# Performance work log

Hardware: AMD Instinct MI355X
Metric: run time of the kernel (lower is better)

Reference implementation:

```python
import jax, jax.numpy as jnp
import numpy as np
from jax import lax

B, T, IN_DIM, HIDDEN = 8, 4096, 1024, 1024


def setup_inputs() -> dict:
    key = jax.random.key(0)
    k_x, k_wd, k_wb = jax.random.split(key, 3)
    x = jax.random.normal(k_x, (B, T, IN_DIM), dtype=jnp.float32)
    h0 = jnp.zeros((B, HIDDEN), dtype=jnp.float32)
    # nn.Linear default init ~ U(-1/sqrt(in), 1/sqrt(in)); b_proj.weight ~ N(0, 0.02)
    lim = 1.0 / np.sqrt(IN_DIM)
    Wd = jax.random.uniform(k_wd, (HIDDEN, IN_DIM), jnp.float32, -lim, lim)
    bd = jnp.zeros((HIDDEN,), dtype=jnp.float32)
    Wb = 0.02 * jax.random.normal(k_wb, (HIDDEN, IN_DIM), dtype=jnp.float32)
    bb = jnp.zeros((HIDDEN,), dtype=jnp.float32)
    # 'hasani' init: A_log = log(linspace(0.5, 2.0, hidden))
    A_log = jnp.log(jnp.linspace(0.5, 2.0, HIDDEN, dtype=jnp.float32))
    return {"x": x, "h0": h0, "Wd": Wd, "bd": bd, "Wb": Wb, "bb": bb, "A_log": A_log}


def _combine(c1, c2):
    # composition of affine maps h -> a*h + b
    a1, b1 = c1
    a2, b2 = c2
    return a1 * a2, a2 * b1 + b2


def reference(x, h0, Wd, bd, Wb, bb, A_log):
    # projections: (B,T,in) @ (in,hidden)
    delta = jax.nn.softplus(jnp.einsum('bti,hi->bth', x, Wd) + bd)
    b_t = delta * (jnp.einsum('bti,hi->bth', x, Wb) + bb)
    A = jnp.exp(A_log)                      # (H,) decay rate
    A_t = jnp.exp(-delta * A)               # (B,T,H)
    # parallel (Blelloch/Heinsen-style) associative scan over T:
    # cumulative affine maps give h_t = A_cum_t * h0 + B_cum_t
    A_cum, B_cum = lax.associative_scan(_combine, (A_t, b_t), axis=1)
    h_full = A_cum * h0[:, None, :] + B_cum  # (B,T,H)
    return jnp.tanh(h_full)                  # bound=True
```

## Files before the change

kernel.cpp:

```cpp
#include <hip/hip_runtime.h>
#include <math.h>

#define B_DIM 8
#define T_DIM 4096
#define K_DIM 1024
#define H_DIM 1024
#define M_DIM (B_DIM * T_DIM)

#define CH 64
#define NC (T_DIM / CH)
#define BK 64
#define NKS (K_DIM / BK)

typedef short bf16x8 __attribute__((ext_vector_type(8)));
typedef float f32x4  __attribute__((ext_vector_type(4)));

__device__ __forceinline__ unsigned short f2bf(float f) {
  unsigned int u = __builtin_bit_cast(unsigned int, f);
  u += 0x7FFFu + ((u >> 16) & 1u);
  return (unsigned short)(u >> 16);
}

__device__ __forceinline__ void gload_lds16(const void* g, void* l) {
  __builtin_amdgcn_global_load_lds(
      (const __attribute__((address_space(1))) unsigned int*)g,
      (__attribute__((address_space(3))) unsigned int*)l,
      16 , 0 , 0 );
}

__device__ __forceinline__ float softplus_fast(float x) {
  float e = __expf(-fabsf(x));
  return fmaxf(x, 0.f) + __logf(1.f + e);
}

__device__ __forceinline__ float tanh_fast(float x) {
  float e = __expf(2.f * x);
  return 1.f - 2.f * __builtin_amdgcn_rcpf(e + 1.f);
}

__global__ __launch_bounds__(256) void k_cvt(const float* __restrict__ in,
                                             unsigned short* __restrict__ out,
                                             int n8) {
  int i = blockIdx.x * 256 + threadIdx.x;
  if (i >= n8) return;
  float4 v0 = ((const float4*)in)[i * 2 + 0];
  float4 v1 = ((const float4*)in)[i * 2 + 1];
  bf16x8 r;
  r[0] = (short)f2bf(v0.x); r[1] = (short)f2bf(v0.y);
  r[2] = (short)f2bf(v0.z); r[3] = (short)f2bf(v0.w);
  r[4] = (short)f2bf(v1.x); r[5] = (short)f2bf(v1.y);
  r[6] = (short)f2bf(v1.z); r[7] = (short)f2bf(v1.w);
  ((bf16x8*)out)[i] = r;
}

#define MFMA_Q(AF, BF, MQ, NQ)                                                 \
  do {                                                                         \
    __builtin_amdgcn_s_setprio(1);                                             \
    _Pragma("unroll")                                                          \
    for (int mm = 0; mm < 4; mm++)                                             \
      _Pragma("unroll")                                                        \
      for (int nn = 0; nn < 2; nn++)                                           \
        _Pragma("unroll")                                                      \
        for (int kk = 0; kk < 2; kk++)                                         \
          acc[(MQ)*4 + mm][(NQ)*2 + nn] =                                      \
              __builtin_amdgcn_mfma_f32_16x16x32_bf16(                         \
                  AF[mm*2 + kk], BF[nn*2 + kk],                                \
                  acc[(MQ)*4 + mm][(NQ)*2 + nn], 0, 0, 0);                     \
    __builtin_amdgcn_s_setprio(0);                                             \
  } while (0)

__global__ __launch_bounds__(512, 2) void k_gemm_dual(
    const unsigned short* __restrict__ Xb,
    const unsigned short* __restrict__ Wdb,
    const unsigned short* __restrict__ Wbb,
    const float* __restrict__ bd,
    const float* __restrict__ bb,
    const float* __restrict__ A_log,
    float* __restrict__ a_out,
    float* __restrict__ b_out,
    float* __restrict__ aggA,
    float* __restrict__ aggB)
{
  __shared__ unsigned short As[2][256 * BK];
  __shared__ unsigned short Bs[2][256 * BK];

  const int tid  = threadIdx.x;
  const int wgid = blockIdx.x;
  const int xcd  = wgid & 7;
  const int j    = wgid >> 3;
  const int bm   = (xcd * 16 + (j >> 3)) * 256;
  const int bn   = (j & 7) * 128;

  const int w    = tid >> 6;
  const int lane = tid & 63;
  const int wm   = (w >> 2) * 128;
  const int wq   = w & 3;
  const int wn   = wq * 64;

  f32x4 acc[8][4];
  const f32x4 z4 = {0.f, 0.f, 0.f, 0.f};
#pragma unroll
  for (int m = 0; m < 8; m++)
#pragma unroll
    for (int n = 0; n < 4; n++) acc[m][n] = z4;

  const int fr = lane & 15;
  const int hi = lane >> 4;

  auto stage = [&](int t, int d) {
    const int k0 = t * BK;
#pragma unroll
    for (int i = 0; i < 4; i++) {
      int idx = i * 512 + tid;
      int row = idx >> 3;
      int cg  = (idx & 7) ^ (row & 7);
      size_t ga = (size_t)(bm + row) * K_DIM + (size_t)(k0 + cg * 8);
      gload_lds16(Xb + ga, (char*)As[d] + idx * 16);
      int h = bn + (row >> 6) * 32 + (row & 31);
      const unsigned short* Wsrc = (row & 32) ? Wbb : Wdb;
      size_t gb = (size_t)h * K_DIM + (size_t)(k0 + cg * 8);
      gload_lds16(Wsrc + gb, (char*)Bs[d] + idx * 16);
    }
  };

  auto readA = [&](int d, int mq, bf16x8* Af) {
#pragma unroll
    for (int mm = 0; mm < 4; mm++) {
      int row = wm + mq * 64 + mm * 16 + fr;
#pragma unroll
      for (int kk = 0; kk < 2; kk++) {
        int ch = (kk * 4 + hi) ^ (row & 7);
        Af[mm * 2 + kk] = *(const bf16x8*)&As[d][row * BK + ch * 8];
      }
    }
  };
  auto readB = [&](int d, int nq, bf16x8* Bf) {
#pragma unroll
    for (int nn = 0; nn < 2; nn++) {
      int vr = wn + nq * 32 + nn * 16 + fr;
#pragma unroll
      for (int kk = 0; kk < 2; kk++) {
        int ch = (kk * 4 + hi) ^ (vr & 7);
        Bf[nn * 2 + kk] = *(const bf16x8*)&Bs[d][vr * BK + ch * 8];
      }
    }
  };

  stage(0, 0);

  bf16x8 A0[8], A1[8], B0[4], B1[4];
#pragma unroll 1
  for (int t = 0; t < NKS; ++t) {
    const int d = t & 1;
    if (t + 1 < NKS) {
      stage(t + 1, d ^ 1);
      asm volatile("s_waitcnt vmcnt(8)" ::: "memory");
    } else {
      asm volatile("s_waitcnt vmcnt(0)" ::: "memory");
    }
    __builtin_amdgcn_s_barrier();

    readA(d, 0, A0); readB(d, 0, B0);
    MFMA_Q(A0, B0, 0, 0);
    __builtin_amdgcn_s_barrier();
    readB(d, 1, B1);
    MFMA_Q(A0, B1, 0, 1);
    __builtin_amdgcn_s_barrier();
    readA(d, 1, A1);
    MFMA_Q(A1, B0, 1, 0);
    __builtin_amdgcn_s_barrier();
    MFMA_Q(A1, B1, 1, 1);
    __builtin_amdgcn_s_barrier();
  }

  const int col   = fr;
  const int rbase = hi * 4;
  const int bidx  = bm >> 12;
  const int cch0  = ((bm + wm) & (T_DIM - 1)) >> 6;

#pragma unroll
  for (int np = 0; np < 2; np++) {
    int gn = bn + wq * 32 + np * 16 + col;
    float bdv = bd[gn];
    float bbv = bb[gn];
    float Ah  = __expf(A_log[gn]);
    float segA[8], segB[8];
#pragma unroll
    for (int m = 0; m < 8; m++) {
      float sA = 1.f, sB = 0.f;
#pragma unroll
      for (int r = 0; r < 4; r++) {
        int gm = bm + wm + m * 16 + rbase + r;
        float z1  = acc[m][np][r] + bdv;
        float z2  = acc[m][np + 2][r] + bbv;
        float dlt = softplus_fast(z1);
        float av  = __expf(-dlt * Ah);
        float bv  = dlt * z2;
        size_t off = (size_t)gm * H_DIM + (size_t)gn;
        a_out[off] = av;
        b_out[off] = bv;
        sB = fmaf(av, sB, bv);
        sA *= av;
      }
      segA[m] = sA; segB[m] = sB;
    }
#pragma unroll
    for (int g = 0; g < 2; g++) {
      float chA = 1.f, chB = 0.f;
#pragma unroll
      for (int mi = 0; mi < 4; mi++) {
        int m = g * 4 + mi;
#pragma unroll
        for (int h2 = 0; h2 < 4; h2++) {
          float sa = __shfl(segA[m], col + h2 * 16, 64);
          float sb = __shfl(segB[m], col + h2 * 16, 64);
          chB = fmaf(sa, chB, sb);
          chA *= sa;
        }
      }
      if (lane < 16) {
        size_t o = ((size_t)(bidx * NC + cch0 + g) << 10) + (size_t)gn;
        aggA[o] = chA;
        aggB[o] = chB;
      }
    }
  }
}

__global__ __launch_bounds__(256) void k_scan_chunks(
    const float* __restrict__ aggA, const float* __restrict__ aggB,
    const float* __restrict__ h0, float* __restrict__ hstart)
{
  int idx = blockIdx.x * 256 + threadIdx.x;
  int h   = idx & (H_DIM - 1);
  int b   = idx >> 10;
  float hc = h0[idx];
  for (int c = 0; c < NC; c++) {
    size_t o = ((size_t)(b * NC + c) << 10) + (size_t)h;
    hstart[o] = hc;
    hc = fmaf(aggA[o], hc, aggB[o]);
  }
}

__global__ __launch_bounds__(256) void k_scan_apply(
    const float* __restrict__ a_arr, const float* b_arr,
    const float* __restrict__ hstart, float* out)
{
  int idx = blockIdx.x * 256 + threadIdx.x;
  int h   = idx & (H_DIM - 1);
  int bc  = idx >> 10;
  int c   = bc & (NC - 1);
  int b   = bc >> 6;
  size_t base = ((size_t)b * T_DIM + (size_t)c * CH) * H_DIM + (size_t)h;
  float hc = hstart[idx];
#pragma unroll 4
  for (int i = 0; i < CH; i++) {
    size_t o = base + (size_t)i * H_DIM;
    float at = a_arr[o];
    float bt = b_arr[o];
    hc = fmaf(at, hc, bt);
    out[o] = tanh_fast(hc);
  }
}

extern "C" void kernel_launch(void* const* d_in, const int* in_sizes, int n_in,
                              void* d_out, int out_size, void* d_ws, size_t ws_size,
                              hipStream_t stream) {
  const float* x     = (const float*)d_in[0];
  const float* h0    = (const float*)d_in[1];
  const float* Wd    = (const float*)d_in[2];
  const float* bd    = (const float*)d_in[3];
  const float* Wb    = (const float*)d_in[4];
  const float* bb    = (const float*)d_in[5];
  const float* A_log = (const float*)d_in[6];
  float* out = (float*)d_out;

  char* ws = (char*)d_ws;
  unsigned short* xb   = (unsigned short*)(ws + 0);
  unsigned short* wdb  = (unsigned short*)(ws + 67108864);
  unsigned short* wbb  = (unsigned short*)(ws + 69206016);
  float*          aarr = (float*)(ws + 71303168);
  float*          aggA = (float*)(ws + 205520896);
  float*          aggB = (float*)(ws + 207618048);
  float*          hst  = (float*)(ws + 209715200);
  float*          barr = out;

  k_cvt<<<(M_DIM * K_DIM / 8) / 256, 256, 0, stream>>>(x, xb, M_DIM * K_DIM / 8);
  k_cvt<<<(H_DIM * K_DIM / 8) / 256, 256, 0, stream>>>(Wd, wdb, H_DIM * K_DIM / 8);
  k_cvt<<<(H_DIM * K_DIM / 8) / 256, 256, 0, stream>>>(Wb, wbb, H_DIM * K_DIM / 8);

  k_gemm_dual<<<(M_DIM / 256) * (H_DIM / 128), 512, 0, stream>>>(
      xb, wdb, wbb, bd, bb, A_log, aarr, barr, aggA, aggB);

  k_scan_chunks<<<(B_DIM * H_DIM) / 256,      256, 0, stream>>>(aggA, aggB, h0, hst);
  k_scan_apply <<<(B_DIM * NC * H_DIM) / 256, 256, 0, stream>>>(aarr, barr, hst, out);
}
```

Before: 357.3 us.

## Interleave next-tile global loads with MFMA quadrants in the GEMM main loop

Splits the next K-tile prefetch into per-chunk A and B loads and spreads them across the four MFMA quadrants of each iteration, rather than issuing them all at the loop top. Adds explicit lgkmcnt(0) waits with sched barriers and fine-grained vmcnt waits so the async global-to-LDS loads complete just before the buffer is consumed. The goal is to hide global-load latency behind compute and avoid bursty memory issue. It adds extra barriers and relies on careful counting of outstanding loads, so a miscount could cause races or stalls.

```diff
diff --git a/kernel.cpp b/kernel.cpp
--- a/kernel.cpp
+++ b/kernel.cpp
@@ -69,6 +69,12 @@
     __builtin_amdgcn_s_setprio(0);                                             \
   } while (0)
 
+#define LGKM0_PIN()                                                            \
+  do {                                                                         \
+    asm volatile("s_waitcnt lgkmcnt(0)" ::: "memory");                         \
+    __builtin_amdgcn_sched_barrier(0);                                         \
+  } while (0)
+
 __global__ __launch_bounds__(512, 2) void k_gemm_dual(
     const unsigned short* __restrict__ Xb,
     const unsigned short* __restrict__ Wdb,
@@ -107,20 +113,21 @@
   const int fr = lane & 15;
   const int hi = lane >> 4;
 
-  auto stage = [&](int t, int d) {
-    const int k0 = t * BK;
-#pragma unroll
-    for (int i = 0; i < 4; i++) {
-      int idx = i * 512 + tid;
-      int row = idx >> 3;
-      int cg  = (idx & 7) ^ (row & 7);
-      size_t ga = (size_t)(bm + row) * K_DIM + (size_t)(k0 + cg * 8);
-      gload_lds16(Xb + ga, (char*)As[d] + idx * 16);
-      int h = bn + (row >> 6) * 32 + (row & 31);
-      const unsigned short* Wsrc = (row & 32) ? Wbb : Wdb;
-      size_t gb = (size_t)h * K_DIM + (size_t)(k0 + cg * 8);
-      gload_lds16(Wsrc + gb, (char*)Bs[d] + idx * 16);
-    }
+  auto stageA = [&](int t, int d, int jj) {
+    int idx = jj * 512 + tid;
+    int row = idx >> 3;
+    int cg  = (idx & 7) ^ (row & 7);
+    size_t ga = (size_t)(bm + row) * K_DIM + (size_t)(t * BK + cg * 8);
+    gload_lds16(Xb + ga, (char*)As[d] + idx * 16);
+  };
+  auto stageB = [&](int t, int d, int jj) {
+    int idx = jj * 512 + tid;
+    int row = idx >> 3;
+    int cg  = (idx & 7) ^ (row & 7);
+    int h = bn + (row >> 6) * 32 + (row & 31);
+    const unsigned short* Wsrc = (row & 32) ? Wbb : Wdb;
+    size_t gb = (size_t)h * K_DIM + (size_t)(t * BK + cg * 8);
+    gload_lds16(Wsrc + gb, (char*)Bs[d] + idx * 16);
   };
 
   auto readA = [&](int d, int mq, bf16x8* Af) {
@@ -146,30 +153,44 @@
     }
   };
 
-  stage(0, 0);
+  stageB(0, 0, 0); stageB(0, 0, 1); stageB(0, 0, 2); stageB(0, 0, 3);
+  stageA(0, 0, 0); stageA(0, 0, 2); stageA(0, 0, 1); stageA(0, 0, 3);
+  asm volatile("s_waitcnt vmcnt(2)" ::: "memory");
+  __builtin_amdgcn_s_barrier();
 
   bf16x8 A0[8], A1[8], B0[4], B1[4];
 #pragma unroll 1
   for (int t = 0; t < NKS; ++t) {
-    const int d = t & 1;
-    if (t + 1 < NKS) {
-      stage(t + 1, d ^ 1);
-      asm volatile("s_waitcnt vmcnt(8)" ::: "memory");
-    } else {
-      asm volatile("s_waitcnt vmcnt(0)" ::: "memory");
-    }
-    __builtin_amdgcn_s_barrier();
+    const int d = t & 1, e = d ^ 1;
+    const bool nxt = (t + 1 < NKS);
 
     readA(d, 0, A0); readB(d, 0, B0);
+    if (nxt) { stageB(t + 1, e, 0); stageB(t + 1, e, 1); }
+    __builtin_amdgcn_s_barrier();
+    LGKM0_PIN();
     MFMA_Q(A0, B0, 0, 0);
     __builtin_amdgcn_s_barrier();
+
     readB(d, 1, B1);
+    if (nxt) { stageB(t + 1, e, 2); stageB(t + 1, e, 3); }
+    __builtin_amdgcn_s_barrier();
+    LGKM0_PIN();
     MFMA_Q(A0, B1, 0, 1);
-    __builtin_amdgcn_s_barrier();
+    if (nxt) asm volatile("s_waitcnt vmcnt(4)" ::: "memory");
+    else     asm volatile("s_waitcnt vmcnt(0)" ::: "memory");
+    __builtin_amdgcn_s_barrier();
+
     readA(d, 1, A1);
+    if (nxt) { stageA(t + 1, e, 0); stageA(t + 1, e, 2); }
+    __builtin_amdgcn_s_barrier();
+    LGKM0_PIN();
     MFMA_Q(A1, B0, 1, 0);
     __builtin_amdgcn_s_barrier();
+
+    if (nxt) { stageA(t + 1, e, 1); stageA(t + 1, e, 3); }
+    __builtin_amdgcn_s_barrier();
     MFMA_Q(A1, B1, 1, 1);
+    if (nxt) asm volatile("s_waitcnt vmcnt(2)" ::: "memory");
     __builtin_amdgcn_s_barrier();
   }
 
```

Result: faster. 329.8 us (-7.7%).

## Restructure GEMM main loop: precomputed addresses, one barrier per tile, unroll by two

Applied to the files above, without the earlier changes.

Rewrites the K-loop of the fused projection GEMM. It precomputes the global and LDS addresses outside the loop and unrolls by two so buffer indices become compile-time constants. It also replaces the four per-tile barriers with a single wait-and-barrier placed after the MFMAs, so the prefetch of the next tile overlaps the current tile's compute. The cost is waiting for all outstanding loads (vmcnt(0)) at the end of each tile instead of a partial wait. That could expose memory latency, and it relies on the next stage being issued before the current buffer is read.

```diff
diff --git a/kernel.cpp b/kernel.cpp
--- a/kernel.cpp
+++ b/kernel.cpp
@@ -107,70 +107,75 @@
   const int fr = lane & 15;
   const int hi = lane >> 4;
 
-  auto stage = [&](int t, int d) {
-    const int k0 = t * BK;
-#pragma unroll
-    for (int i = 0; i < 4; i++) {
-      int idx = i * 512 + tid;
-      int row = idx >> 3;
-      int cg  = (idx & 7) ^ (row & 7);
-      size_t ga = (size_t)(bm + row) * K_DIM + (size_t)(k0 + cg * 8);
-      gload_lds16(Xb + ga, (char*)As[d] + idx * 16);
-      int h = bn + (row >> 6) * 32 + (row & 31);
-      const unsigned short* Wsrc = (row & 32) ? Wbb : Wdb;
-      size_t gb = (size_t)h * K_DIM + (size_t)(k0 + cg * 8);
-      gload_lds16(Wsrc + gb, (char*)Bs[d] + idx * 16);
-    }
-  };
-
-  auto readA = [&](int d, int mq, bf16x8* Af) {
-#pragma unroll
-    for (int mm = 0; mm < 4; mm++) {
-      int row = wm + mq * 64 + mm * 16 + fr;
-#pragma unroll
-      for (int kk = 0; kk < 2; kk++) {
-        int ch = (kk * 4 + hi) ^ (row & 7);
-        Af[mm * 2 + kk] = *(const bf16x8*)&As[d][row * BK + ch * 8];
-      }
-    }
-  };
-  auto readB = [&](int d, int nq, bf16x8* Bf) {
-#pragma unroll
-    for (int nn = 0; nn < 2; nn++) {
-      int vr = wn + nq * 32 + nn * 16 + fr;
-#pragma unroll
-      for (int kk = 0; kk < 2; kk++) {
-        int ch = (kk * 4 + hi) ^ (vr & 7);
-        Bf[nn * 2 + kk] = *(const bf16x8*)&Bs[d][vr * BK + ch * 8];
-      }
-    }
-  };
-
-  stage(0, 0);
-
-  bf16x8 A0[8], A1[8], B0[4], B1[4];
+  const unsigned short* gA[4];
+  const unsigned short* gB[4];
+  int ldsoff[4];
+#pragma unroll
+  for (int jj = 0; jj < 4; jj++) {
+    int idx = jj * 512 + tid;
+    int row = idx >> 3;
+    int cg  = (idx & 7) ^ (row & 7);
+    ldsoff[jj] = idx * 16;
+    gA[jj] = Xb + (size_t)(bm + row) * K_DIM + (size_t)(cg * 8);
+    int h = bn + (row >> 6) * 32 + (row & 31);
+    const unsigned short* Wsrc = (row & 32) ? Wbb : Wdb;
+    gB[jj] = Wsrc + (size_t)h * K_DIM + (size_t)(cg * 8);
+  }
+
+#define STAGE(T, D)                                                           \
+  do {                                                                        \
+    _Pragma("unroll")                                                         \
+    for (int jj = 0; jj < 4; jj++) {                                          \
+      gload_lds16(gA[jj] + (T) * BK, (char*)As[D] + ldsoff[jj]);              \
+      gload_lds16(gB[jj] + (T) * BK, (char*)Bs[D] + ldsoff[jj]);              \
+    }                                                                         \
+  } while (0)
+
+  const int ch0 = hi ^ (fr & 7);
+  const int ch1 = ch0 ^ 4;
+  const char* bA0 = (const char*)As + (size_t)((wm + fr) * 128 + ch0 * 16);
+  const char* bA1 = (const char*)As + (size_t)((wm + fr) * 128 + ch1 * 16);
+  const char* bB0 = (const char*)Bs + (size_t)((wn + fr) * 128 + ch0 * 16);
+  const char* bB1 = (const char*)Bs + (size_t)((wn + fr) * 128 + ch1 * 16);
+
+#define RDA(DST, D, MQ)                                                       \
+  _Pragma("unroll")                                                           \
+  for (int mm = 0; mm < 4; mm++) {                                            \
+    DST[mm*2+0] = *(const bf16x8*)(bA0 + (D)*32768 + ((MQ)*64 + mm*16)*128);  \
+    DST[mm*2+1] = *(const bf16x8*)(bA1 + (D)*32768 + ((MQ)*64 + mm*16)*128);  \
+  }
+#define RDB(DST, D, NQ)                                                       \
+  _Pragma("unroll")                                                           \
+  for (int nn = 0; nn < 2; nn++) {                                            \
+    DST[nn*2+0] = *(const bf16x8*)(bB0 + (D)*32768 + ((NQ)*32 + nn*16)*128);  \
+    DST[nn*2+1] = *(const bf16x8*)(bB1 + (D)*32768 + ((NQ)*32 + nn*16)*128);  \
+  }
+
+#define TILE(T, D, NXT)                                                       \
+  do {                                                                        \
+    if (NXT) STAGE((T) + 1, (D) ^ 1);                                         \
+    bf16x8 A0[8], A1[8], B0[4], B1[4];                                        \
+    RDA(A0, D, 0); RDB(B0, D, 0);                                             \
+    MFMA_Q(A0, B0, 0, 0);                                                     \
+    RDB(B1, D, 1);                                                            \
+    MFMA_Q(A0, B1, 0, 1);                                                     \
+    RDA(A1, D, 1);                                                            \
+    MFMA_Q(A1, B0, 1, 0);                                                     \
+    MFMA_Q(A1, B1, 1, 1);                                                     \
+    if (NXT) {                                                                \
+      asm volatile("s_waitcnt vmcnt(0)" ::: "memory");                        \
+      __builtin_amdgcn_s_barrier();                                           \
+    }                                                                         \
+  } while (0)
+
+  STAGE(0, 0);
+  asm volatile("s_waitcnt vmcnt(0)" ::: "memory");
+  __builtin_amdgcn_s_barrier();
+
 #pragma unroll 1
-  for (int t = 0; t < NKS; ++t) {
-    const int d = t & 1;
-    if (t + 1 < NKS) {
-      stage(t + 1, d ^ 1);
-      asm volatile("s_waitcnt vmcnt(8)" ::: "memory");
-    } else {
-      asm volatile("s_waitcnt vmcnt(0)" ::: "memory");
-    }
-    __builtin_amdgcn_s_barrier();
-
-    readA(d, 0, A0); readB(d, 0, B0);
-    MFMA_Q(A0, B0, 0, 0);
-    __builtin_amdgcn_s_barrier();
-    readB(d, 1, B1);
-    MFMA_Q(A0, B1, 0, 1);
-    __builtin_amdgcn_s_barrier();
-    readA(d, 1, A1);
-    MFMA_Q(A1, B0, 1, 0);
-    __builtin_amdgcn_s_barrier();
-    MFMA_Q(A1, B1, 1, 1);
-    __builtin_amdgcn_s_barrier();
+  for (int t = 0; t < NKS; t += 2) {
+    TILE(t,     0, true);
+    TILE(t + 1, 1, (t + 2) < NKS);
   }
 
   const int col   = fr;
```

New measurement: 336.1 us. -5.9%, faster.
